# Kernel tuning notes

Measured on AMD Instinct MI355X. Metric: run time of the kernel, lower is better.

Reference implementation:

```python
import jax, jax.numpy as jnp
import numpy as np
import math

RCR = 5.2
NUM_SPECIES = 7
AEV_DIM = 1008
WIDTHS = [1008, 256, 192, 160]


def setup_inputs() -> dict:
    key = jax.random.key(0)
    ks = jax.random.split(key, 12)
    B, N = 1, 2048
    species = jax.random.randint(ks[0], (B, N), 0, NUM_SPECIES, dtype=jnp.int64 if jax.config.read('jax_enable_x64') else jnp.int32)
    coordinates = jax.random.uniform(ks[1], (B, N, 3), dtype=jnp.float32) * 6.0
    EtaR = jnp.array([16.0], dtype=jnp.float32)
    ShfR = jnp.array([0.9 + 0.18 * x for x in range(16)], dtype=jnp.float32)
    s = 0.05
    W0 = jax.random.normal(ks[2], (NUM_SPECIES, WIDTHS[1], WIDTHS[0]), jnp.float32) * s
    b0 = jax.random.normal(ks[3], (NUM_SPECIES, WIDTHS[1]), jnp.float32) * s
    W1 = jax.random.normal(ks[4], (NUM_SPECIES, WIDTHS[2], WIDTHS[1]), jnp.float32) * s
    b1 = jax.random.normal(ks[5], (NUM_SPECIES, WIDTHS[2]), jnp.float32) * s
    W2 = jax.random.normal(ks[6], (NUM_SPECIES, WIDTHS[3], WIDTHS[2]), jnp.float32) * s
    b2 = jax.random.normal(ks[7], (NUM_SPECIES, WIDTHS[3]), jnp.float32) * s
    Wf = jax.random.normal(ks[8], (NUM_SPECIES, 1, WIDTHS[3]), jnp.float32) * s
    bf = jax.random.normal(ks[9], (NUM_SPECIES, 1), jnp.float32) * s
    return {'species': species, 'coordinates': coordinates, 'EtaR': EtaR, 'ShfR': ShfR,
            'W0': W0, 'b0': b0, 'W1': W1, 'b1': b1, 'W2': W2, 'b2': b2, 'Wf': Wf, 'bf': bf}


def _celu(x, alpha=0.1):
    return jnp.maximum(x, 0.0) + jnp.minimum(0.0, alpha * jnp.expm1(x / alpha))


def _aev(species, coordinates, EtaR, ShfR):
    B, N = species.shape
    diff = coordinates[:, :, None, :] - coordinates[:, None, :, :]  # [B,N,N,3]
    dsq = jnp.sum(diff * diff, axis=-1)
    safe = jnp.where(dsq > 0, dsq, 1.0)
    dist = jnp.sqrt(safe)  # [B,N,N], diag is a dummy 1.0
    mask = (dsq > 0) & (dist <= RCR)
    fc = (0.5 * jnp.cos(math.pi * dist / RCR) + 0.5) * mask.astype(jnp.float32)
    onehot = jax.nn.one_hot(species, NUM_SPECIES, dtype=jnp.float32)  # [B,N,S]
    core = jnp.exp(-EtaR[0] * (dist[..., None] - ShfR) ** 2)  # [B,N,N,R]
    weighted = core * fc[..., None]
    # sum over neighbor j, grouped by neighbor species s (species-major concat order)
    radial = jnp.einsum('bijr,bjs->bisr', weighted, onehot)  # [B,N,S,R]
    radial = radial.reshape(B, N, NUM_SPECIES * ShfR.shape[0])
    pad = AEV_DIM - radial.shape[-1]
    return jnp.pad(radial, ((0, 0), (0, 0), (0, pad)))


def reference(species, coordinates, EtaR, ShfR, W0, b0, W1, b1, W2, b2, Wf, bf):
    aev = _aev(species, coordinates, EtaR, ShfR)  # [B,N,1008]
    # run all 7 element nets on every atom (matches the module's redundant-compute semantics)
    h = _celu(jnp.einsum('soh,bnh->sbno', W0, aev) + b0[:, None, None, :])
    h = _celu(jnp.einsum('soh,sbnh->sbno', W1, h) + b1[:, None, None, :])
    h = _celu(jnp.einsum('soh,sbnh->sbno', W2, h) + b2[:, None, None, :])
    e = jnp.einsum('soh,sbnh->sbno', Wf, h) + bf[:, None, None, :]  # [S,B,N,1]
    onehot = jax.nn.one_hot(species, NUM_SPECIES, dtype=jnp.float32)  # [B,N,S]
    total = jnp.einsum('sbn,bns->', e[..., 0], onehot)
    return total.reshape(1)
```

## Files before the change

kernel.cpp:

```cpp
#include <hip/hip_runtime.h>

#define N_ATOMS 2048
#define NSPEC 7
#define NR 16
#define NFEAT 112
#define RCR_F 5.2f
#define H0 256
#define H1 192
#define H2 160
#define W0_PITCH 1008
#define TILE 8
#define NTILES (N_ATOMS / TILE)

#define WS_SEG     0
#define WS_SCOORD  16384
#define WS_AEV     65536
#define WS_H0BUF   1048576
#define WS_H1BUF   3145728

__device__ __forceinline__ float celu01(float x) {
    return x > 0.f ? x : 0.1f * (__expf(x * 10.f) - 1.f);
}

__global__ __launch_bounds__(256) void sort_kernel(const int* __restrict__ species,
                                                   const float* __restrict__ coords,
                                                   int* __restrict__ seg,
                                                   float4* __restrict__ scoord,
                                                   float* __restrict__ out) {
    __shared__ int cnt[NSPEC];
    __shared__ int cur[NSPEC];
    int t = threadIdx.x;
    if (t < NSPEC) cnt[t] = 0;
    __syncthreads();
    for (int a = t; a < N_ATOMS; a += 256) atomicAdd(&cnt[species[a]], 1);
    __syncthreads();
    if (t == 0) {
        int run = 0;
        for (int s = 0; s < NSPEC; s++) { seg[s] = run; cur[s] = run; run += cnt[s]; }
        seg[NSPEC] = run;
        out[0] = 0.0f;
    }
    __syncthreads();
    for (int a = t; a < N_ATOMS; a += 256) {
        int sp = species[a];
        int pos = atomicAdd(&cur[sp], 1);
        scoord[pos] = make_float4(coords[3*a], coords[3*a+1], coords[3*a+2], 0.f);
    }
}

__global__ __launch_bounds__(128) void aev_kernel(const float4* __restrict__ scoord,
                                                  const int* __restrict__ seg,
                                                  const float* __restrict__ ShfR,
                                                  const float* __restrict__ EtaR,
                                                  float* __restrict__ aev) {
    int p = blockIdx.x;
    int L = threadIdx.x;
    int s = L >> 4, c = L & 15;
    float4 ci = scoord[p];
    float eta = EtaR[0];
    float shf[NR];
#pragma unroll
    for (int r = 0; r < NR; r++) shf[r] = ShfR[r];
    float acc[NR];
#pragma unroll
    for (int r = 0; r < NR; r++) acc[r] = 0.f;

    int kbeg = 0, kend = 0;
    if (s < NSPEC) { kbeg = seg[s] + c; kend = seg[s + 1]; }
    const float rc2 = RCR_F * RCR_F;
    const float cosk = 3.14159265358979f / RCR_F;

    for (int k = kbeg; k < kend; k += 16) {
        float4 cj = scoord[k];
        float dx = ci.x - cj.x, dy = ci.y - cj.y, dz = ci.z - cj.z;
        float dsq = dx*dx + dy*dy + dz*dz;
        bool valid = (dsq > 0.f) && (dsq <= rc2);
        float d = sqrtf(dsq);
        float fc = 0.5f * __cosf(d * cosk) + 0.5f;
        fc = valid ? fc : 0.f;
#pragma unroll
        for (int r = 0; r < NR; r++) {
            float u = d - shf[r];
            acc[r] = fmaf(__expf(-eta * u * u), fc, acc[r]);
        }
    }
#pragma unroll
    for (int r = 0; r < NR; r++) {
        float v = acc[r];
        v += __shfl_xor(v, 1);
        v += __shfl_xor(v, 2);
        v += __shfl_xor(v, 4);
        v += __shfl_xor(v, 8);
        acc[r] = v;
    }
    if (s < NSPEC && c == 0) {
        float* dst = aev + p * NFEAT + s * NR;
#pragma unroll
        for (int r = 0; r < NR; r += 4)
            *(float4*)(dst + r) = make_float4(acc[r], acc[r+1], acc[r+2], acc[r+3]);
    }
}


__global__ __launch_bounds__(512) void mlp0_kernel(const float* __restrict__ W0,
                                                   const float* __restrict__ b0,
                                                   const float* __restrict__ aev,
                                                   const int* __restrict__ seg,
                                                   float* __restrict__ h0out) {
    __shared__ float4 hs[TILE * (NFEAT / 4)];
    int s = blockIdx.y;
    int base = seg[s] + blockIdx.x * TILE;
    int segend = seg[s + 1];
    if (base >= segend) return;
    int n_act = min(TILE, segend - base);

    int t = threadIdx.x;
    {
        const float4* src = (const float4*)(aev + (size_t)base * NFEAT);
        int nfl4 = min(TILE * (NFEAT / 4), (N_ATOMS - base) * (NFEAT / 4));
        for (int j = t; j < nfl4; j += 512) hs[j] = src[j];
    }
    __syncthreads();

    int o = t >> 1, ks = t & 1;
    const float* Wrow = W0 + (size_t)(s * H0 + o) * W0_PITCH + ks * 4;
    float bias = b0[s * H0 + o];
    float acc[TILE];
#pragma unroll
    for (int q = 0; q < TILE; q++) acc[q] = 0.f;

#pragma unroll 7
    for (int i = 0; i < NFEAT / 8; i++) {
        float4 w = *(const float4*)(Wrow + i * 8);
#pragma unroll
        for (int q = 0; q < TILE; q++) {
            float4 a = hs[q * (NFEAT / 4) + i * 2 + ks];
            acc[q] += w.x*a.x + w.y*a.y + w.z*a.z + w.w*a.w;
        }
    }
#pragma unroll
    for (int q = 0; q < TILE; q++) {
        float v = acc[q];
        v += __shfl_xor(v, 1);
        if (ks == 0 && q < n_act)
            h0out[(size_t)(base + q) * H0 + o] = celu01(v + bias);
    }
}

__global__ __launch_bounds__(768) void mlp1_kernel(const float* __restrict__ W1,
                                                   const float* __restrict__ b1,
                                                   const float* __restrict__ h0,
                                                   const int* __restrict__ seg,
                                                   float* __restrict__ h1out) {
    __shared__ float4 hs[TILE * (H0 / 4)];
    int s = blockIdx.y;
    int base = seg[s] + blockIdx.x * TILE;
    int segend = seg[s + 1];
    if (base >= segend) return;
    int n_act = min(TILE, segend - base);

    int t = threadIdx.x;
    {
        const float4* src = (const float4*)(h0 + (size_t)base * H0);
        int nfl4 = min(TILE * (H0 / 4), (N_ATOMS - base) * (H0 / 4));
        for (int j = t; j < nfl4; j += 768) hs[j] = src[j];
    }
    __syncthreads();

    int o = t >> 2, ks = t & 3;
    const float* Wrow = W1 + (size_t)(s * H1 + o) * H0 + ks * 4;
    float bias = b1[s * H1 + o];
    float acc[TILE];
#pragma unroll
    for (int q = 0; q < TILE; q++) acc[q] = 0.f;

#pragma unroll 4
    for (int i = 0; i < H0 / 16; i++) {
        float4 w = *(const float4*)(Wrow + i * 16);
#pragma unroll
        for (int q = 0; q < TILE; q++) {
            float4 a = hs[q * (H0 / 4) + i * 4 + ks];
            acc[q] += w.x*a.x + w.y*a.y + w.z*a.z + w.w*a.w;
        }
    }
#pragma unroll
    for (int q = 0; q < TILE; q++) {
        float v = acc[q];
        v += __shfl_xor(v, 1);
        v += __shfl_xor(v, 2);
        if (ks == 0 && q < n_act)
            h1out[(size_t)(base + q) * H1 + o] = celu01(v + bias);
    }
}

__global__ __launch_bounds__(640) void mlp2_kernel(const float* __restrict__ W2,
                                                   const float* __restrict__ b2,
                                                   const float* __restrict__ Wf,
                                                   const float* __restrict__ bf,
                                                   const float* __restrict__ h1,
                                                   const int* __restrict__ seg,
                                                   float* __restrict__ out) {
    __shared__ float4 hs[TILE * (H1 / 4)];
    __shared__ float bsum;
    int s = blockIdx.y;
    int base = seg[s] + blockIdx.x * TILE;
    int segend = seg[s + 1];
    if (base >= segend) return;
    int n_act = min(TILE, segend - base);

    int t = threadIdx.x;
    if (t == 0) bsum = 0.f;
    {
        const float4* src = (const float4*)(h1 + (size_t)base * H1);
        int nfl4 = min(TILE * (H1 / 4), (N_ATOMS - base) * (H1 / 4));
        for (int j = t; j < nfl4; j += 640) hs[j] = src[j];
    }
    __syncthreads();

    int o = t >> 2, ks = t & 3;
    const float* Wrow = W2 + (size_t)(s * H2 + o) * H1 + ks * 4;
    float bias = b2[s * H2 + o];
    float wf = Wf[s * H2 + o];
    float acc[TILE];
#pragma unroll
    for (int q = 0; q < TILE; q++) acc[q] = 0.f;

#pragma unroll 4
    for (int i = 0; i < H1 / 16; i++) {
        float4 w = *(const float4*)(Wrow + i * 16);
#pragma unroll
        for (int q = 0; q < TILE; q++) {
            float4 a = hs[q * (H1 / 4) + i * 4 + ks];
            acc[q] += w.x*a.x + w.y*a.y + w.z*a.z + w.w*a.w;
        }
    }
    float contrib = 0.f;
#pragma unroll
    for (int q = 0; q < TILE; q++) {
        float v = acc[q];
        v += __shfl_xor(v, 1);
        v += __shfl_xor(v, 2);
        if (ks == 0 && q < n_act)
            contrib += wf * celu01(v + bias);
    }
    if (t == 0) contrib += (float)n_act * bf[s];

    float v = contrib;
    v += __shfl_down(v, 32);
    v += __shfl_down(v, 16);
    v += __shfl_down(v, 8);
    v += __shfl_down(v, 4);
    v += __shfl_down(v, 2);
    v += __shfl_down(v, 1);
    if ((t & 63) == 0) atomicAdd(&bsum, v);
    __syncthreads();
    if (t == 0) atomicAdd(out, bsum);
}

extern "C" void kernel_launch(void* const* d_in, const int* in_sizes, int n_in,
                              void* d_out, int out_size, void* d_ws, size_t ws_size,
                              hipStream_t stream) {
    const int*   species = (const int*)d_in[0];
    const float* coords  = (const float*)d_in[1];
    const float* EtaR    = (const float*)d_in[2];
    const float* ShfR    = (const float*)d_in[3];
    const float* W0      = (const float*)d_in[4];
    const float* b0      = (const float*)d_in[5];
    const float* W1      = (const float*)d_in[6];
    const float* b1      = (const float*)d_in[7];
    const float* W2      = (const float*)d_in[8];
    const float* b2      = (const float*)d_in[9];
    const float* Wf      = (const float*)d_in[10];
    const float* bf      = (const float*)d_in[11];
    float* out = (float*)d_out;
    char* ws = (char*)d_ws;

    int*    seg    = (int*)(ws + WS_SEG);
    float4* scoord = (float4*)(ws + WS_SCOORD);
    float*  aev    = (float*)(ws + WS_AEV);
    float*  h0buf  = (float*)(ws + WS_H0BUF);
    float*  h1buf  = (float*)(ws + WS_H1BUF);

    hipLaunchKernelGGL(sort_kernel, dim3(1), dim3(256), 0, stream,
                       species, coords, seg, scoord, out);
    hipLaunchKernelGGL(aev_kernel, dim3(N_ATOMS), dim3(128), 0, stream,
                       scoord, seg, ShfR, EtaR, aev);
    hipLaunchKernelGGL(mlp0_kernel, dim3(NTILES, NSPEC), dim3(512), 0, stream,
                       W0, b0, aev, seg, h0buf);
    hipLaunchKernelGGL(mlp1_kernel, dim3(NTILES, NSPEC), dim3(768), 0, stream,
                       W1, b1, h0buf, seg, h1buf);
    hipLaunchKernelGGL(mlp2_kernel, dim3(NTILES, NSPEC), dim3(640), 0, stream,
                       W2, b2, Wf, bf, h1buf, seg, out);
}
```

Baseline: 153.1 us.

## Fuse AEV computation and three MLP layers into one kernel per atom tile

Replaces the separate AEV kernel and three MLP-layer kernels with a single kernel. Each block computes AEVs for its tile of 8 atoms, one wave per atom, with 8 lanes per neighbor species. It then runs all three layers with intermediates held in shared memory. This removes three kernel launches and the global-memory round trips for the AEV, h0 and h1 buffers. In exchange, AEV work per block is serialized over 8 lanes per species instead of 16, and the whole chain runs at the occupancy of a 512-thread block.

New measurement: 178.6 us. 16.7% more time.

```diff
diff --git a/kernel.cpp b/kernel.cpp
--- a/kernel.cpp
+++ b/kernel.cpp
@@ -14,9 +14,6 @@
 
 #define WS_SEG     0
 #define WS_SCOORD  16384
-#define WS_AEV     65536
-#define WS_H0BUF   1048576
-#define WS_H1BUF   3145728
 
 __device__ __forceinline__ float celu01(float x) {
     return x > 0.f ? x : 0.1f * (__expf(x * 10.f) - 1.f);
@@ -48,200 +45,155 @@
     }
 }
 
-__global__ __launch_bounds__(128) void aev_kernel(const float4* __restrict__ scoord,
-                                                  const int* __restrict__ seg,
-                                                  const float* __restrict__ ShfR,
-                                                  const float* __restrict__ EtaR,
-                                                  float* __restrict__ aev) {
-    int p = blockIdx.x;
-    int L = threadIdx.x;
-    int s = L >> 4, c = L & 15;
-    float4 ci = scoord[p];
-    float eta = EtaR[0];
-    float shf[NR];
-#pragma unroll
-    for (int r = 0; r < NR; r++) shf[r] = ShfR[r];
-    float acc[NR];
-#pragma unroll
-    for (int r = 0; r < NR; r++) acc[r] = 0.f;
-
-    int kbeg = 0, kend = 0;
-    if (s < NSPEC) { kbeg = seg[s] + c; kend = seg[s + 1]; }
-    const float rc2 = RCR_F * RCR_F;
-    const float cosk = 3.14159265358979f / RCR_F;
-
-    for (int k = kbeg; k < kend; k += 16) {
-        float4 cj = scoord[k];
-        float dx = ci.x - cj.x, dy = ci.y - cj.y, dz = ci.z - cj.z;
-        float dsq = dx*dx + dy*dy + dz*dz;
-        bool valid = (dsq > 0.f) && (dsq <= rc2);
-        float d = sqrtf(dsq);
-        float fc = 0.5f * __cosf(d * cosk) + 0.5f;
-        fc = valid ? fc : 0.f;
-#pragma unroll
-        for (int r = 0; r < NR; r++) {
-            float u = d - shf[r];
-            acc[r] = fmaf(__expf(-eta * u * u), fc, acc[r]);
-        }
-    }
-#pragma unroll
-    for (int r = 0; r < NR; r++) {
-        float v = acc[r];
-        v += __shfl_xor(v, 1);
-        v += __shfl_xor(v, 2);
-        v += __shfl_xor(v, 4);
-        v += __shfl_xor(v, 8);
-        acc[r] = v;
-    }
-    if (s < NSPEC && c == 0) {
-        float* dst = aev + p * NFEAT + s * NR;
-#pragma unroll
-        for (int r = 0; r < NR; r += 4)
-            *(float4*)(dst + r) = make_float4(acc[r], acc[r+1], acc[r+2], acc[r+3]);
-    }
-}
-
-
-__global__ __launch_bounds__(512) void mlp0_kernel(const float* __restrict__ W0,
-                                                   const float* __restrict__ b0,
-                                                   const float* __restrict__ aev,
-                                                   const int* __restrict__ seg,
-                                                   float* __restrict__ h0out) {
-    __shared__ float4 hs[TILE * (NFEAT / 4)];
+__global__ __launch_bounds__(512) void fused_kernel(const float4* __restrict__ scoord,
+                                                    const int* __restrict__ seg,
+                                                    const float* __restrict__ ShfR,
+                                                    const float* __restrict__ EtaR,
+                                                    const float* __restrict__ W0,
+                                                    const float* __restrict__ b0,
+                                                    const float* __restrict__ W1,
+                                                    const float* __restrict__ b1,
+                                                    const float* __restrict__ W2,
+                                                    const float* __restrict__ b2,
+                                                    const float* __restrict__ Wf,
+                                                    const float* __restrict__ bf,
+                                                    float* __restrict__ out) {
+    __shared__ float aevs[TILE][NFEAT];
+    __shared__ float h0s[TILE][H0];
+    __shared__ float h1s[TILE][H1];
+    __shared__ float bsum;
+
     int s = blockIdx.y;
+    int segend = seg[s + 1];
     int base = seg[s] + blockIdx.x * TILE;
-    int segend = seg[s + 1];
     if (base >= segend) return;
     int n_act = min(TILE, segend - base);
 
     int t = threadIdx.x;
+    if (t == 0) bsum = 0.f;
+
     {
-        const float4* src = (const float4*)(aev + (size_t)base * NFEAT);
-        int nfl4 = min(TILE * (NFEAT / 4), (N_ATOMS - base) * (NFEAT / 4));
-        for (int j = t; j < nfl4; j += 512) hs[j] = src[j];
+        int w = t >> 6, lane = t & 63;
+        int p = base + (w < n_act ? w : 0);
+        int sA = lane >> 3, c = lane & 7;
+        float4 ci = scoord[p];
+        float eta = EtaR[0];
+        float shf[NR];
+#pragma unroll
+        for (int r = 0; r < NR; r++) shf[r] = ShfR[r];
+        float acc[NR];
+#pragma unroll
+        for (int r = 0; r < NR; r++) acc[r] = 0.f;
+
+        int kbeg = 0, kend = 0;
+        if (sA < NSPEC) { kbeg = seg[sA] + c; kend = seg[sA + 1]; }
+        const float rc2 = RCR_F * RCR_F;
+        const float cosk = 3.14159265358979f / RCR_F;
+
+        for (int k = kbeg; k < kend; k += 8) {
+            float4 cj = scoord[k];
+            float dx = ci.x - cj.x, dy = ci.y - cj.y, dz = ci.z - cj.z;
+            float dsq = dx*dx + dy*dy + dz*dz;
+            bool valid = (dsq > 0.f) && (dsq <= rc2);
+            float d = sqrtf(dsq);
+            float fc = 0.5f * __cosf(d * cosk) + 0.5f;
+            fc = valid ? fc : 0.f;
+#pragma unroll
+            for (int r = 0; r < NR; r++) {
+                float u = d - shf[r];
+                acc[r] = fmaf(__expf(-eta * u * u), fc, acc[r]);
+            }
+        }
+#pragma unroll
+        for (int r = 0; r < NR; r++) {
+            float v = acc[r];
+            v += __shfl_xor(v, 1);
+            v += __shfl_xor(v, 2);
+            v += __shfl_xor(v, 4);
+            acc[r] = v;
+        }
+        if (sA < NSPEC && c == 0) {
+            float* dst = &aevs[w][sA * NR];
+#pragma unroll
+            for (int r = 0; r < NR; r += 4)
+                *(float4*)(dst + r) = make_float4(acc[r], acc[r+1], acc[r+2], acc[r+3]);
+        }
     }
     __syncthreads();
 
     int o = t >> 1, ks = t & 1;
-    const float* Wrow = W0 + (size_t)(s * H0 + o) * W0_PITCH + ks * 4;
-    float bias = b0[s * H0 + o];
-    float acc[TILE];
-#pragma unroll
-    for (int q = 0; q < TILE; q++) acc[q] = 0.f;
-
+
+    {
+        const float* Wr = W0 + (size_t)(s * H0 + o) * W0_PITCH + ks * 4;
+        float bias = b0[s * H0 + o];
+        float acc[TILE];
+#pragma unroll
+        for (int q = 0; q < TILE; q++) acc[q] = 0.f;
 #pragma unroll 7
-    for (int i = 0; i < NFEAT / 8; i++) {
-        float4 w = *(const float4*)(Wrow + i * 8);
+        for (int i = 0; i < NFEAT / 8; i++) {
+            float4 w = *(const float4*)(Wr + i * 8);
+#pragma unroll
+            for (int q = 0; q < TILE; q++) {
+                float4 a = *(const float4*)(&aevs[q][i * 8 + ks * 4]);
+                acc[q] += w.x*a.x + w.y*a.y + w.z*a.z + w.w*a.w;
+            }
+        }
 #pragma unroll
         for (int q = 0; q < TILE; q++) {
-            float4 a = hs[q * (NFEAT / 4) + i * 2 + ks];
-            acc[q] += w.x*a.x + w.y*a.y + w.z*a.z + w.w*a.w;
-        }
-    }
-#pragma unroll
-    for (int q = 0; q < TILE; q++) {
-        float v = acc[q];
-        v += __shfl_xor(v, 1);
-        if (ks == 0 && q < n_act)
-            h0out[(size_t)(base + q) * H0 + o] = celu01(v + bias);
-    }
-}
-
-__global__ __launch_bounds__(768) void mlp1_kernel(const float* __restrict__ W1,
-                                                   const float* __restrict__ b1,
-                                                   const float* __restrict__ h0,
-                                                   const int* __restrict__ seg,
-                                                   float* __restrict__ h1out) {
-    __shared__ float4 hs[TILE * (H0 / 4)];
-    int s = blockIdx.y;
-    int base = seg[s] + blockIdx.x * TILE;
-    int segend = seg[s + 1];
-    if (base >= segend) return;
-    int n_act = min(TILE, segend - base);
-
-    int t = threadIdx.x;
-    {
-        const float4* src = (const float4*)(h0 + (size_t)base * H0);
-        int nfl4 = min(TILE * (H0 / 4), (N_ATOMS - base) * (H0 / 4));
-        for (int j = t; j < nfl4; j += 768) hs[j] = src[j];
-    }
-    __syncthreads();
-
-    int o = t >> 2, ks = t & 3;
-    const float* Wrow = W1 + (size_t)(s * H1 + o) * H0 + ks * 4;
-    float bias = b1[s * H1 + o];
-    float acc[TILE];
-#pragma unroll
-    for (int q = 0; q < TILE; q++) acc[q] = 0.f;
-
+            float v = acc[q];
+            v += __shfl_xor(v, 1);
+            if (ks == 0) h0s[q][o] = celu01(v + bias);
+        }
+    }
+    __syncthreads();
+
+    if (o < H1) {
+        const float* Wr = W1 + (size_t)(s * H1 + o) * H0 + ks * 4;
+        float bias = b1[s * H1 + o];
+        float acc[TILE];
+#pragma unroll
+        for (int q = 0; q < TILE; q++) acc[q] = 0.f;
 #pragma unroll 4
-    for (int i = 0; i < H0 / 16; i++) {
-        float4 w = *(const float4*)(Wrow + i * 16);
+        for (int i = 0; i < H0 / 8; i++) {
+            float4 w = *(const float4*)(Wr + i * 8);
+#pragma unroll
+            for (int q = 0; q < TILE; q++) {
+                float4 a = *(const float4*)(&h0s[q][i * 8 + ks * 4]);
+                acc[q] += w.x*a.x + w.y*a.y + w.z*a.z + w.w*a.w;
+            }
+        }
 #pragma unroll
         for (int q = 0; q < TILE; q++) {
-            float4 a = hs[q * (H0 / 4) + i * 4 + ks];
-            acc[q] += w.x*a.x + w.y*a.y + w.z*a.z + w.w*a.w;
-        }
-    }
-#pragma unroll
-    for (int q = 0; q < TILE; q++) {
-        float v = acc[q];
-        v += __shfl_xor(v, 1);
-        v += __shfl_xor(v, 2);
-        if (ks == 0 && q < n_act)
-            h1out[(size_t)(base + q) * H1 + o] = celu01(v + bias);
-    }
-}
-
-__global__ __launch_bounds__(640) void mlp2_kernel(const float* __restrict__ W2,
-                                                   const float* __restrict__ b2,
-                                                   const float* __restrict__ Wf,
-                                                   const float* __restrict__ bf,
-                                                   const float* __restrict__ h1,
-                                                   const int* __restrict__ seg,
-                                                   float* __restrict__ out) {
-    __shared__ float4 hs[TILE * (H1 / 4)];
-    __shared__ float bsum;
-    int s = blockIdx.y;
-    int base = seg[s] + blockIdx.x * TILE;
-    int segend = seg[s + 1];
-    if (base >= segend) return;
-    int n_act = min(TILE, segend - base);
-
-    int t = threadIdx.x;
-    if (t == 0) bsum = 0.f;
-    {
-        const float4* src = (const float4*)(h1 + (size_t)base * H1);
-        int nfl4 = min(TILE * (H1 / 4), (N_ATOMS - base) * (H1 / 4));
-        for (int j = t; j < nfl4; j += 640) hs[j] = src[j];
-    }
-    __syncthreads();
-
-    int o = t >> 2, ks = t & 3;
-    const float* Wrow = W2 + (size_t)(s * H2 + o) * H1 + ks * 4;
-    float bias = b2[s * H2 + o];
-    float wf = Wf[s * H2 + o];
-    float acc[TILE];
-#pragma unroll
-    for (int q = 0; q < TILE; q++) acc[q] = 0.f;
-
+            float v = acc[q];
+            v += __shfl_xor(v, 1);
+            if (ks == 0) h1s[q][o] = celu01(v + bias);
+        }
+    }
+    __syncthreads();
+
+    float contrib = 0.f;
+    if (o < H2) {
+        const float* Wr = W2 + (size_t)(s * H2 + o) * H1 + ks * 4;
+        float bias = b2[s * H2 + o];
+        float wf = Wf[s * H2 + o];
+        float acc[TILE];
+#pragma unroll
+        for (int q = 0; q < TILE; q++) acc[q] = 0.f;
 #pragma unroll 4
-    for (int i = 0; i < H1 / 16; i++) {
-        float4 w = *(const float4*)(Wrow + i * 16);
+        for (int i = 0; i < H1 / 8; i++) {
+            float4 w = *(const float4*)(Wr + i * 8);
+#pragma unroll
+            for (int q = 0; q < TILE; q++) {
+                float4 a = *(const float4*)(&h1s[q][i * 8 + ks * 4]);
+                acc[q] += w.x*a.x + w.y*a.y + w.z*a.z + w.w*a.w;
+            }
+        }
 #pragma unroll
         for (int q = 0; q < TILE; q++) {
-            float4 a = hs[q * (H1 / 4) + i * 4 + ks];
-            acc[q] += w.x*a.x + w.y*a.y + w.z*a.z + w.w*a.w;
-        }
-    }
-    float contrib = 0.f;
-#pragma unroll
-    for (int q = 0; q < TILE; q++) {
-        float v = acc[q];
-        v += __shfl_xor(v, 1);
-        v += __shfl_xor(v, 2);
-        if (ks == 0 && q < n_act)
-            contrib += wf * celu01(v + bias);
+            float v = acc[q];
+            v += __shfl_xor(v, 1);
+            if (ks == 0 && q < n_act) contrib += wf * celu01(v + bias);
+        }
     }
     if (t == 0) contrib += (float)n_act * bf[s];
 
@@ -277,18 +229,9 @@
 
     int*    seg    = (int*)(ws + WS_SEG);
     float4* scoord = (float4*)(ws + WS_SCOORD);
-    float*  aev    = (float*)(ws + WS_AEV);
-    float*  h0buf  = (float*)(ws + WS_H0BUF);
-    float*  h1buf  = (float*)(ws + WS_H1BUF);
 
     hipLaunchKernelGGL(sort_kernel, dim3(1), dim3(256), 0, stream,
                        species, coords, seg, scoord, out);
-    hipLaunchKernelGGL(aev_kernel, dim3(N_ATOMS), dim3(128), 0, stream,
-                       scoord, seg, ShfR, EtaR, aev);
-    hipLaunchKernelGGL(mlp0_kernel, dim3(NTILES, NSPEC), dim3(512), 0, stream,
-                       W0, b0, aev, seg, h0buf);
-    hipLaunchKernelGGL(mlp1_kernel, dim3(NTILES, NSPEC), dim3(768), 0, stream,
-                       W1, b1, h0buf, seg, h1buf);
-    hipLaunchKernelGGL(mlp2_kernel, dim3(NTILES, NSPEC), dim3(640), 0, stream,
-                       W2, b2, Wf, bf, h1buf, seg, out);
-}
+    hipLaunchKernelGGL(fused_kernel, dim3(NTILES, NSPEC), dim3(512), 0, stream,
+                       scoord, seg, ShfR, EtaR, W0, b0, W1, b1, W2, b2, Wf, bf, out);
+}
```

## Remap AEV to one wavefront per atom-species and drop MLP shared staging

Applied to the files above, without the earlier changes.

The AEV kernel now gives each (atom, neighbour species) pair its own 64-lane wavefront through a 2D grid, replacing one 128-thread block per atom in which a 16-lane group handled each species and one group sat idle. The MLP kernels no longer stage activations into shared memory and read them straight from global memory, relying on L1/L2 broadcast. mlp0 now uses 1024 threads with a 4-way K split. The aim is to cut idle lanes and barrier overhead, at the cost of more redundant global loads of the activations and, in the AEV kernel, more blocks and longer shuffle reductions.

Measured after the change: 242.5 us. 58.5% more time.

```diff
diff --git a/kernel.cpp b/kernel.cpp
--- a/kernel.cpp
+++ b/kernel.cpp
@@ -48,14 +48,15 @@
     }
 }
 
-__global__ __launch_bounds__(128) void aev_kernel(const float4* __restrict__ scoord,
+__global__ __launch_bounds__(256) void aev_kernel(const float4* __restrict__ scoord,
                                                   const int* __restrict__ seg,
                                                   const float* __restrict__ ShfR,
                                                   const float* __restrict__ EtaR,
                                                   float* __restrict__ aev) {
-    int p = blockIdx.x;
-    int L = threadIdx.x;
-    int s = L >> 4, c = L & 15;
+    int s = blockIdx.y;
+    int p = blockIdx.x * 4 + (threadIdx.x >> 6);
+    int lane = threadIdx.x & 63;
+
     float4 ci = scoord[p];
     float eta = EtaR[0];
     float shf[NR];
@@ -65,12 +66,12 @@
 #pragma unroll
     for (int r = 0; r < NR; r++) acc[r] = 0.f;
 
-    int kbeg = 0, kend = 0;
-    if (s < NSPEC) { kbeg = seg[s] + c; kend = seg[s + 1]; }
+    int kbeg = seg[s] + lane;
+    int kend = seg[s + 1];
     const float rc2 = RCR_F * RCR_F;
     const float cosk = 3.14159265358979f / RCR_F;
 
-    for (int k = kbeg; k < kend; k += 16) {
+    for (int k = kbeg; k < kend; k += 64) {
         float4 cj = scoord[k];
         float dx = ci.x - cj.x, dy = ci.y - cj.y, dz = ci.z - cj.z;
         float dsq = dx*dx + dy*dy + dz*dz;
@@ -91,10 +92,12 @@
         v += __shfl_xor(v, 2);
         v += __shfl_xor(v, 4);
         v += __shfl_xor(v, 8);
+        v += __shfl_xor(v, 16);
+        v += __shfl_xor(v, 32);
         acc[r] = v;
     }
-    if (s < NSPEC && c == 0) {
-        float* dst = aev + p * NFEAT + s * NR;
+    if (lane == 0) {
+        float* dst = aev + (size_t)p * NFEAT + s * NR;
 #pragma unroll
         for (int r = 0; r < NR; r += 4)
             *(float4*)(dst + r) = make_float4(acc[r], acc[r+1], acc[r+2], acc[r+3]);
@@ -102,39 +105,31 @@
 }
 
 
-__global__ __launch_bounds__(512) void mlp0_kernel(const float* __restrict__ W0,
-                                                   const float* __restrict__ b0,
-                                                   const float* __restrict__ aev,
-                                                   const int* __restrict__ seg,
-                                                   float* __restrict__ h0out) {
-    __shared__ float4 hs[TILE * (NFEAT / 4)];
-    int s = blockIdx.y;
+__global__ __launch_bounds__(1024) void mlp0_kernel(const float* __restrict__ W0,
+                                                    const float* __restrict__ b0,
+                                                    const float* __restrict__ aev,
+                                                    const int* __restrict__ seg,
+                                                    float* __restrict__ h0out) {
+    int s = blockIdx.y;
+    int segend = seg[s + 1];
     int base = seg[s] + blockIdx.x * TILE;
-    int segend = seg[s + 1];
     if (base >= segend) return;
     int n_act = min(TILE, segend - base);
 
     int t = threadIdx.x;
-    {
-        const float4* src = (const float4*)(aev + (size_t)base * NFEAT);
-        int nfl4 = min(TILE * (NFEAT / 4), (N_ATOMS - base) * (NFEAT / 4));
-        for (int j = t; j < nfl4; j += 512) hs[j] = src[j];
-    }
-    __syncthreads();
-
-    int o = t >> 1, ks = t & 1;
-    const float* Wrow = W0 + (size_t)(s * H0 + o) * W0_PITCH + ks * 4;
+    int o = t >> 2, ks = t & 3;
+    const float* Wr = W0 + (size_t)(s * H0 + o) * W0_PITCH + ks * 4;
     float bias = b0[s * H0 + o];
     float acc[TILE];
 #pragma unroll
     for (int q = 0; q < TILE; q++) acc[q] = 0.f;
 
-#pragma unroll 7
-    for (int i = 0; i < NFEAT / 8; i++) {
-        float4 w = *(const float4*)(Wrow + i * 8);
+#pragma unroll
+    for (int i = 0; i < NFEAT / 16; i++) {
+        float4 w = *(const float4*)(Wr + i * 16);
 #pragma unroll
         for (int q = 0; q < TILE; q++) {
-            float4 a = hs[q * (NFEAT / 4) + i * 2 + ks];
+            float4 a = *(const float4*)(aev + (size_t)(base + q) * NFEAT + i * 16 + ks * 4);
             acc[q] += w.x*a.x + w.y*a.y + w.z*a.z + w.w*a.w;
         }
     }
@@ -142,6 +137,7 @@
     for (int q = 0; q < TILE; q++) {
         float v = acc[q];
         v += __shfl_xor(v, 1);
+        v += __shfl_xor(v, 2);
         if (ks == 0 && q < n_act)
             h0out[(size_t)(base + q) * H0 + o] = celu01(v + bias);
     }
@@ -152,23 +148,15 @@
                                                    const float* __restrict__ h0,
                                                    const int* __restrict__ seg,
                                                    float* __restrict__ h1out) {
-    __shared__ float4 hs[TILE * (H0 / 4)];
-    int s = blockIdx.y;
+    int s = blockIdx.y;
+    int segend = seg[s + 1];
     int base = seg[s] + blockIdx.x * TILE;
-    int segend = seg[s + 1];
     if (base >= segend) return;
     int n_act = min(TILE, segend - base);
 
     int t = threadIdx.x;
-    {
-        const float4* src = (const float4*)(h0 + (size_t)base * H0);
-        int nfl4 = min(TILE * (H0 / 4), (N_ATOMS - base) * (H0 / 4));
-        for (int j = t; j < nfl4; j += 768) hs[j] = src[j];
-    }
-    __syncthreads();
-
     int o = t >> 2, ks = t & 3;
-    const float* Wrow = W1 + (size_t)(s * H1 + o) * H0 + ks * 4;
+    const float* Wr = W1 + (size_t)(s * H1 + o) * H0 + ks * 4;
     float bias = b1[s * H1 + o];
     float acc[TILE];
 #pragma unroll
@@ -176,10 +164,10 @@
 
 #pragma unroll 4
     for (int i = 0; i < H0 / 16; i++) {
-        float4 w = *(const float4*)(Wrow + i * 16);
+        float4 w = *(const float4*)(Wr + i * 16);
 #pragma unroll
         for (int q = 0; q < TILE; q++) {
-            float4 a = hs[q * (H0 / 4) + i * 4 + ks];
+            float4 a = *(const float4*)(h0 + (size_t)(base + q) * H0 + i * 16 + ks * 4);
             acc[q] += w.x*a.x + w.y*a.y + w.z*a.z + w.w*a.w;
         }
     }
@@ -200,25 +188,19 @@
                                                    const float* __restrict__ h1,
                                                    const int* __restrict__ seg,
                                                    float* __restrict__ out) {
-    __shared__ float4 hs[TILE * (H1 / 4)];
     __shared__ float bsum;
     int s = blockIdx.y;
+    int segend = seg[s + 1];
     int base = seg[s] + blockIdx.x * TILE;
-    int segend = seg[s + 1];
     if (base >= segend) return;
     int n_act = min(TILE, segend - base);
 
     int t = threadIdx.x;
     if (t == 0) bsum = 0.f;
-    {
-        const float4* src = (const float4*)(h1 + (size_t)base * H1);
-        int nfl4 = min(TILE * (H1 / 4), (N_ATOMS - base) * (H1 / 4));
-        for (int j = t; j < nfl4; j += 640) hs[j] = src[j];
-    }
     __syncthreads();
 
     int o = t >> 2, ks = t & 3;
-    const float* Wrow = W2 + (size_t)(s * H2 + o) * H1 + ks * 4;
+    const float* Wr = W2 + (size_t)(s * H2 + o) * H1 + ks * 4;
     float bias = b2[s * H2 + o];
     float wf = Wf[s * H2 + o];
     float acc[TILE];
@@ -227,10 +209,10 @@
 
 #pragma unroll 4
     for (int i = 0; i < H1 / 16; i++) {
-        float4 w = *(const float4*)(Wrow + i * 16);
+        float4 w = *(const float4*)(Wr + i * 16);
 #pragma unroll
         for (int q = 0; q < TILE; q++) {
-            float4 a = hs[q * (H1 / 4) + i * 4 + ks];
+            float4 a = *(const float4*)(h1 + (size_t)(base + q) * H1 + i * 16 + ks * 4);
             acc[q] += w.x*a.x + w.y*a.y + w.z*a.z + w.w*a.w;
         }
     }
@@ -240,8 +222,7 @@
         float v = acc[q];
         v += __shfl_xor(v, 1);
         v += __shfl_xor(v, 2);
-        if (ks == 0 && q < n_act)
-            contrib += wf * celu01(v + bias);
+        if (ks == 0 && q < n_act) contrib += wf * celu01(v + bias);
     }
     if (t == 0) contrib += (float)n_act * bf[s];
 
@@ -283,9 +264,9 @@
 
     hipLaunchKernelGGL(sort_kernel, dim3(1), dim3(256), 0, stream,
                        species, coords, seg, scoord, out);
-    hipLaunchKernelGGL(aev_kernel, dim3(N_ATOMS), dim3(128), 0, stream,
+    hipLaunchKernelGGL(aev_kernel, dim3(N_ATOMS / 4, NSPEC), dim3(256), 0, stream,
                        scoord, seg, ShfR, EtaR, aev);
-    hipLaunchKernelGGL(mlp0_kernel, dim3(NTILES, NSPEC), dim3(512), 0, stream,
+    hipLaunchKernelGGL(mlp0_kernel, dim3(NTILES, NSPEC), dim3(1024), 0, stream,
                        W0, b0, aev, seg, h0buf);
     hipLaunchKernelGGL(mlp1_kernel, dim3(NTILES, NSPEC), dim3(768), 0, stream,
                        W1, b1, h0buf, seg, h1buf);
```
